# Performance work log

Measured on AMD Instinct MI355X. Metric: run time of the kernel, lower is better.

Reference implementation:

```python
import jax, jax.numpy as jnp
import numpy as np

D_MODEL = 1024
N_HEADS = 16


def setup_inputs() -> dict:
    key = jax.random.key(0)
    ks = jax.random.split(key, 7)
    scale = 1.0 / np.sqrt(D_MODEL)
    seq = jax.random.normal(ks[0], (4, 1024, D_MODEL), dtype=jnp.float32)
    Wq = jax.random.normal(ks[1], (D_MODEL, D_MODEL), dtype=jnp.float32) * scale
    bq = jax.random.normal(ks[2], (D_MODEL,), dtype=jnp.float32) * 0.02
    Wk = jax.random.normal(ks[3], (D_MODEL, D_MODEL), dtype=jnp.float32) * scale
    bk = jax.random.normal(ks[4], (D_MODEL,), dtype=jnp.float32) * 0.02
    Wv = jax.random.normal(ks[5], (D_MODEL, D_MODEL), dtype=jnp.float32) * scale
    bv = jax.random.normal(ks[6], (D_MODEL,), dtype=jnp.float32) * 0.02
    return {"seq": seq, "Wq": Wq, "bq": bq, "Wk": Wk, "bk": bk, "Wv": Wv, "bv": bv}


def reference(seq, Wq, bq, Wk, bk, Wv, bv):
    B, S, D = seq.shape
    H = N_HEADS
    dv = D // H
    # nn.Linear: x @ W.T + b; W stored [out, in]
    q = (seq @ Wq.T + bq).reshape(B, S, H, dv).transpose(0, 2, 1, 3)  # [B,H,S,dv]
    k = (seq @ Wk.T + bk).reshape(B, S, H, dv).transpose(0, 2, 1, 3)
    v = (seq @ Wv.T + bv).reshape(B, S, H, dv).transpose(0, 2, 1, 3)
    scores = jnp.einsum('bhqd,bhkd->bhqk', q, k) / jnp.sqrt(jnp.asarray(dv, seq.dtype))
    p = jax.nn.softmax(scores, axis=-1)
    out = jnp.einsum('bhqk,bhkd->bhqd', p, v)  # [B,H,S,dv]
    return out.transpose(0, 2, 1, 3).reshape(B, S, D)
```

## Files before the change

kernel.cpp:

```cpp
#include <hip/hip_runtime.h>
#include <hip/hip_fp16.h>

typedef _Float16 f16x8 __attribute__((ext_vector_type(8)));
typedef _Float16 f16x4 __attribute__((ext_vector_type(4)));
typedef float f32x4 __attribute__((ext_vector_type(4)));

#define D_MODEL 1024
#define SEQ 1024
#define BATCH 4
#define NH 16
#define DV 64
#define M_TOTAL (BATCH * SEQ)
#define QBLK 128

__device__ __forceinline__ void gload16(const _Float16* g, _Float16* lds) {
    __builtin_amdgcn_global_load_lds((const __attribute__((address_space(1))) void*)g,
                                     (__attribute__((address_space(3))) void*)lds,
                                     16, 0, 0);
}

__global__ void cvt_f32_f16(const float* __restrict__ s, _Float16* __restrict__ d, int n) {
    int i = (blockIdx.x * blockDim.x + threadIdx.x) * 8;
    if (i >= n) return;
    float4 a = *(const float4*)(s + i);
    float4 b = *(const float4*)(s + i + 4);
    f16x8 h;
    h[0] = (_Float16)a.x; h[1] = (_Float16)a.y; h[2] = (_Float16)a.z; h[3] = (_Float16)a.w;
    h[4] = (_Float16)b.x; h[5] = (_Float16)b.y; h[6] = (_Float16)b.z; h[7] = (_Float16)b.w;
    *(f16x8*)(d + i) = h;
}

__global__ void cvt3_f32_f16(const float* __restrict__ s0, const float* __restrict__ s1,
                             const float* __restrict__ s2, _Float16* __restrict__ d0,
                             _Float16* __restrict__ d1, _Float16* __restrict__ d2, int n) {
    const float* s = (blockIdx.y == 0) ? s0 : (blockIdx.y == 1 ? s1 : s2);
    _Float16*    d = (blockIdx.y == 0) ? d0 : (blockIdx.y == 1 ? d1 : d2);
    int i = (blockIdx.x * blockDim.x + threadIdx.x) * 8;
    if (i >= n) return;
    float4 a = *(const float4*)(s + i);
    float4 b = *(const float4*)(s + i + 4);
    f16x8 h;
    h[0] = (_Float16)a.x; h[1] = (_Float16)a.y; h[2] = (_Float16)a.z; h[3] = (_Float16)a.w;
    h[4] = (_Float16)b.x; h[5] = (_Float16)b.y; h[6] = (_Float16)b.z; h[7] = (_Float16)b.w;
    *(f16x8*)(d + i) = h;
}

__global__ __launch_bounds__(512, 2) void qkv_gemm(
    const _Float16* __restrict__ X,
    const _Float16* __restrict__ W0, const _Float16* __restrict__ W1, const _Float16* __restrict__ W2,
    const float* __restrict__ b0, const float* __restrict__ b1, const float* __restrict__ b2,
    _Float16* __restrict__ Qo, _Float16* __restrict__ Ko, _Float16* __restrict__ Vto)
{
    __shared__ _Float16 SM[4 * 256 * 64];
#define ABASE(buf) (SM + (buf) * 16384)
#define BBASE(buf) (SM + 32768 + (buf) * 16384)

    const int tid = threadIdx.x;
    const int l = tid & 63;
    const int w = tid >> 6;
    const int wr = w >> 2, wc = w & 3;

    const int bid = blockIdx.x;
    const int nid = (bid & 7) * 24 + (bid >> 3);
    const int mt = nid & 15, ntg = nid >> 4;
    const int mat = ntg >> 2, nt = ntg & 3;
    const _Float16* Wm  = (mat == 0) ? W0 : (mat == 1 ? W1 : W2);
    const float*    bia = (mat == 0) ? b0 : (mat == 1 ? b1 : b2);
    const int m0 = mt * 256, n0 = nt * 256;

    const int str = tid >> 3;
    const int sc8 = ((tid & 7) ^ (str & 7)) * 8;
    const _Float16* xsrc = X  + (size_t)(m0 + str) * D_MODEL + sc8;
    const _Float16* wsrc = Wm + (size_t)(n0 + str) * D_MODEL + sc8;
    const int ldst = str * 64 + (tid & 7) * 8;

#define SA(buf, kt, h) do { \
    gload16(xsrc + (size_t)((h) * 128) * D_MODEL + (kt) * 64, ABASE(buf) + (h) * 8192 + ldst); \
    gload16(xsrc + (size_t)((h) * 128 + 64) * D_MODEL + (kt) * 64, ABASE(buf) + (h) * 8192 + 4096 + ldst); } while (0)
#define SB(buf, kt, h) do { \
    gload16(wsrc + (size_t)((h) * 128) * D_MODEL + (kt) * 64, BBASE(buf) + (h) * 8192 + ldst); \
    gload16(wsrc + (size_t)((h) * 128 + 64) * D_MODEL + (kt) * 64, BBASE(buf) + (h) * 8192 + 4096 + ldst); } while (0)

    const int fr = l & 15, g = l >> 4, fr7 = l & 7;
    const int wrow = wr * 128, bcol = wc * 64;

    f32x4 acc[8][4] = {};
    f16x8 b[4][2];

    SB(0, 0, 0); SB(0, 0, 1);
    SA(0, 0, 0); SA(0, 0, 1);
    SB(1, 1, 0); SB(1, 1, 1);
    asm volatile("s_waitcnt vmcnt(4)" ::: "memory");
    __builtin_amdgcn_s_barrier();

#define PHASES(BUF, TSA_BUF, TSA, TSB_BUF, TSB)                                              \
    _Pragma("unroll")                                                                        \
    for (int p = 0; p < 4; ++p) {                                                            \
        if (p == 0) {                                                                        \
            _Pragma("unroll")                                                                \
            for (int nj = 0; nj < 4; ++nj) {                                                 \
                const int rb = (bcol + nj * 16 + fr) * 64;                                   \
                b[nj][0] = *(const f16x8*)&BBASE(BUF)[rb + ((g ^ fr7) << 3)];                \
                b[nj][1] = *(const f16x8*)&BBASE(BUF)[rb + (((4 + g) ^ fr7) << 3)];          \
            }                                                                                \
        }                                                                                    \
        f16x8 aq[2][2];                                                                      \
        _Pragma("unroll")                                                                    \
        for (int q = 0; q < 2; ++q) {                                                        \
            const int ra = (wrow + (2 * p + q) * 16 + fr) * 64;                              \
            aq[q][0] = *(const f16x8*)&ABASE(BUF)[ra + ((g ^ fr7) << 3)];                    \
            aq[q][1] = *(const f16x8*)&ABASE(BUF)[ra + (((4 + g) ^ fr7) << 3)];              \
        }                                                                                    \
        if (p == 0) SA(TSA_BUF, TSA, 0);                                                     \
        else if (p == 1) SA(TSA_BUF, TSA, 1);                                                \
        else if (p == 2) SB(TSB_BUF, TSB, 0);                                                \
        else SB(TSB_BUF, TSB, 1);                                                            \
        __builtin_amdgcn_s_barrier();                                                        \
        __builtin_amdgcn_s_setprio(1);                                                       \
        _Pragma("unroll")                                                                    \
        for (int ks = 0; ks < 2; ++ks)                                                       \
            _Pragma("unroll")                                                                \
            for (int q = 0; q < 2; ++q)                                                      \
                _Pragma("unroll")                                                            \
                for (int nj = 0; nj < 4; ++nj)                                               \
                    acc[2 * p + q][nj] = __builtin_amdgcn_mfma_f32_16x16x32_f16(             \
                        aq[q][ks], b[nj][ks], acc[2 * p + q][nj], 0, 0, 0);                  \
        __builtin_amdgcn_s_setprio(0);                                                       \
        if (p == 3) asm volatile("s_waitcnt vmcnt(4)" ::: "memory");                         \
        __builtin_amdgcn_s_barrier();                                                        \
    }

    for (int it = 0; it < 8; ++it) {
        const int tA = 2 * it + 1;
        const int tN = (2 * it + 2 < 16) ? 2 * it + 2 : 15;
        const int tM = (2 * it + 3 < 16) ? 2 * it + 3 : 15;
        PHASES(0, 1, tA, 0, tN)
        PHASES(1, 0, tN, 1, tM)
    }
#undef PHASES
#undef SA
#undef SB

    if (mat != 2) {
        const float scale = (mat == 0) ? 0.125f * 1.44269504088896340736f : 1.0f;
#pragma unroll
        for (int nj = 0; nj < 4; ++nj) {
            const int o = n0 + bcol + nj * 16 + fr;
            const float bb = bia[o];
            const int h = o >> 6, dd = o & 63;
#pragma unroll
            for (int mi = 0; mi < 8; ++mi) {
#pragma unroll
                for (int r = 0; r < 4; ++r) {
                    const int m = m0 + wrow + mi * 16 + g * 4 + r;
                    const int bi = m >> 10, s = m & 1023;
                    const float v = (acc[mi][nj][r] + bb) * scale;
                    const _Float16 hv = (_Float16)v;
                    const int bh = bi * NH + h;
                    if (mat == 0) Qo[((size_t)bh * SEQ + s) * DV + dd] = hv;
                    else          Ko[((size_t)bh * SEQ + s) * DV + dd] = hv;
                }
            }
        }
    } else {
        asm volatile("s_waitcnt vmcnt(0)" ::: "memory");
        __syncthreads();
#pragma unroll
        for (int nj = 0; nj < 4; ++nj) {
            const int n = bcol + nj * 16 + fr;
            const float bb = bia[n0 + n];
#pragma unroll
            for (int mi = 0; mi < 8; ++mi) {
#pragma unroll
                for (int r = 0; r < 4; ++r) {
                    const int m = wrow + mi * 16 + g * 4 + r;
                    SM[n * 256 + ((((m >> 3) + n) & 31) << 3) + (m & 7)] =
                        (_Float16)(acc[mi][nj][r] + bb);
                }
            }
        }
        __syncthreads();
        const int bi = m0 >> 10, s0 = m0 & 1023;
#pragma unroll
        for (int itp = 0; itp < 16; ++itp) {
            const int task = itp * 512 + tid;
            const int dd = task >> 5, sc = task & 31;
            f16x8 vv = *(const f16x8*)&SM[dd * 256 + (((sc + dd) & 31) << 3)];
            const int og = n0 + dd;
            const int h = og >> 6, d = og & 63;
            const int bh = bi * NH + h;
            *(f16x8*)(Vto + ((size_t)bh * DV + d) * SEQ + s0 + sc * 8) = vv;
        }
    }
#undef ABASE
#undef BBASE
}

__global__ __launch_bounds__(512, 4) void attn(
    const _Float16* __restrict__ Q, const _Float16* __restrict__ K,
    const _Float16* __restrict__ Vt, float* __restrict__ out)
{
    __shared__ _Float16 Kb[2][64 * 64];
    __shared__ _Float16 Vb[2][64 * 64];
    __shared__ _Float16 P[8][16][80];

    const int tid = threadIdx.x;
    const int w = tid >> 6, l = tid & 63;
    const int qc = l & 15, g = l >> 4;

    const int fid = blockIdx.y * 8 + blockIdx.x;
    const int nid = (fid & 7) * 64 + (fid >> 3);
    const int bh = nid >> 3, qt = nid & 7;
    const int b = bh >> 4, h = bh & 15;
    const int q0 = qt * QBLK + w * 16;

    const int str = tid >> 3;
    const int scs = ((tid & 7) ^ (str & 7)) * 8;
    const int ldst = str * 64 + (tid & 7) * 8;
    const _Float16* Kg = K  + (size_t)bh * SEQ * DV;
    const _Float16* Vg = Vt + (size_t)bh * DV * SEQ;

    const _Float16* qp = Q + ((size_t)bh * SEQ + q0 + qc) * DV + g * 8;
    f16x8 qf0 = *(const f16x8*)(qp);
    f16x8 qf1 = *(const f16x8*)(qp + 32);

    float m_run = -1e30f, l_run = 0.f;
    f32x4 oacc[4] = {};

#define STAGE(buf, kb) do {                                                  \
        gload16(Kg + (size_t)((kb) + str) * DV + scs, &Kb[buf][0] + ldst);   \
        gload16(Vg + (size_t)str * SEQ + (kb) + scs, &Vb[buf][0] + ldst);    \
    } while (0)

    STAGE(0, 0);
    __syncthreads();

    for (int kt = 0; kt < 16; ++kt) {
        const int ct = kt & 1;
        if (kt < 15) STAGE(ct ^ 1, (kt + 1) * 64);
        const _Float16* Ktile = Kb[ct];
        const _Float16* Vtile = Vb[ct];

        f32x4 sT[4];
        const f32x4 zf = {0.f, 0.f, 0.f, 0.f};
        __builtin_amdgcn_s_setprio(1);
#pragma unroll
        for (int kf = 0; kf < 4; ++kf) {
            const int row = kf * 16 + qc;
            f16x8 ka0 = *(const f16x8*)&Ktile[row * 64 + (((g)     ^ (qc & 7)) << 3)];
            f16x8 ka1 = *(const f16x8*)&Ktile[row * 64 + (((4 + g) ^ (qc & 7)) << 3)];
            f32x4 t = __builtin_amdgcn_mfma_f32_16x16x32_f16(ka0, qf0, zf, 0, 0, 0);
            sT[kf] = __builtin_amdgcn_mfma_f32_16x16x32_f16(ka1, qf1, t, 0, 0, 0);
        }
        __builtin_amdgcn_s_setprio(0);

        f32x4 mx = sT[0];
#pragma unroll
        for (int kf = 1; kf < 4; ++kf)
#pragma unroll
            for (int r = 0; r < 4; ++r) mx[r] = fmaxf(mx[r], sT[kf][r]);
        float pmax = fmaxf(fmaxf(mx[0], mx[1]), fmaxf(mx[2], mx[3]));
        pmax = fmaxf(pmax, __shfl_xor(pmax, 16));
        pmax = fmaxf(pmax, __shfl_xor(pmax, 32));
        if (!__all(pmax - m_run <= 8.0f)) {
            const float mn = fmaxf(m_run, pmax);
            const float al = exp2f(m_run - mn);
            l_run *= al;
#pragma unroll
            for (int df = 0; df < 4; ++df) oacc[df] *= al;
            m_run = mn;
        }
        float rsum = 0.f;
#pragma unroll
        for (int kf = 0; kf < 4; ++kf) {
            f16x4 ph;
#pragma unroll
            for (int r = 0; r < 4; ++r) {
                const float p = exp2f(sT[kf][r] - m_run);
                rsum += p;
                ph[r] = (_Float16)p;
            }
            *(f16x4*)&P[w][qc][kf * 16 + g * 4] = ph;
        }
        rsum += __shfl_xor(rsum, 16);
        rsum += __shfl_xor(rsum, 32);
        l_run += rsum;

        __builtin_amdgcn_s_setprio(1);
#pragma unroll
        for (int ks = 0; ks < 2; ++ks) {
            f16x8 pb = *(const f16x8*)&P[w][qc][ks * 32 + g * 8];
#pragma unroll
            for (int df = 0; df < 4; ++df) {
                const int row = df * 16 + qc;
                f16x8 va = *(const f16x8*)&Vtile[row * 64 + (((ks * 4 + g) ^ (qc & 7)) << 3)];
                oacc[df] = __builtin_amdgcn_mfma_f32_16x16x32_f16(va, pb, oacc[df], 0, 0, 0);
            }
        }
        __builtin_amdgcn_s_setprio(0);

        __syncthreads();
    }
#undef STAGE

    const float inv = 1.0f / l_run;
    float* ob = out + ((size_t)b * SEQ + q0 + qc) * D_MODEL + h * DV;
#pragma unroll
    for (int df = 0; df < 4; ++df) {
        float4 v4;
        v4.x = oacc[df][0] * inv; v4.y = oacc[df][1] * inv;
        v4.z = oacc[df][2] * inv; v4.w = oacc[df][3] * inv;
        *(float4*)(ob + df * 16 + g * 4) = v4;
    }
}

extern "C" void kernel_launch(void* const* d_in, const int* in_sizes, int n_in,
                              void* d_out, int out_size, void* d_ws, size_t ws_size,
                              hipStream_t stream) {
    const float* seq = (const float*)d_in[0];
    const float* Wq  = (const float*)d_in[1];
    const float* bq  = (const float*)d_in[2];
    const float* Wk  = (const float*)d_in[3];
    const float* bk  = (const float*)d_in[4];
    const float* Wv  = (const float*)d_in[5];
    const float* bv  = (const float*)d_in[6];
    float* out = (float*)d_out;

    _Float16* seqh = (_Float16*)d_ws;
    _Float16* wqh  = seqh + (size_t)M_TOTAL * D_MODEL;
    _Float16* wkh  = wqh + (size_t)D_MODEL * D_MODEL;
    _Float16* wvh  = wkh + (size_t)D_MODEL * D_MODEL;
    _Float16* Qh   = wvh + (size_t)D_MODEL * D_MODEL;
    _Float16* Kh   = Qh + (size_t)M_TOTAL * D_MODEL;
    _Float16* Vth  = Kh + (size_t)M_TOTAL * D_MODEL;

    const int n_seq = M_TOTAL * D_MODEL;
    const int n_w   = D_MODEL * D_MODEL;
    cvt_f32_f16<<<n_seq / (256 * 8), 256, 0, stream>>>(seq, seqh, n_seq);
    cvt3_f32_f16<<<dim3(n_w / (256 * 8), 3), 256, 0, stream>>>(Wq, Wk, Wv, wqh, wkh, wvh, n_w);

    qkv_gemm<<<192, 512, 0, stream>>>(
        seqh, wqh, wkh, wvh, bq, bk, bv, Qh, Kh, Vth);

    attn<<<dim3(SEQ / QBLK, BATCH * NH), 512, 0, stream>>>(Qh, Kh, Vth, out);
}
```

Before: 84.31 us.

## Software-pipeline attention loop: overlap next QK^T with current softmax/PV using triple buffering

Restructures the attention inner loop so the QK^T MFMAs for tile t+1 are issued before the softmax and PV for tile t, using two score register sets and a three-slot K/V LDS ring. The aim is to hide the latency of exp, reductions and LDS round trips behind matrix-core work, and to keep loads two tiles ahead. In exchange it uses more LDS (an extra K and V buffer) and more registers for the second score set, which may reduce occupancy under launch_bounds(512,4). It also adds explicit vmcnt(0) waits before each barrier.

After: 82.46 us. 2.2% less time.

```diff
diff --git a/kernel.cpp b/kernel.cpp
--- a/kernel.cpp
+++ b/kernel.cpp
@@ -200,8 +200,8 @@
     const _Float16* __restrict__ Q, const _Float16* __restrict__ K,
     const _Float16* __restrict__ Vt, float* __restrict__ out)
 {
-    __shared__ _Float16 Kb[2][64 * 64];
-    __shared__ _Float16 Vb[2][64 * 64];
+    __shared__ _Float16 Kb[3][64 * 64];
+    __shared__ _Float16 Vb[3][64 * 64];
     __shared__ _Float16 P[8][16][80];
 
     const int tid = threadIdx.x;
@@ -226,82 +226,104 @@
 
     float m_run = -1e30f, l_run = 0.f;
     f32x4 oacc[4] = {};
-
-#define STAGE(buf, kb) do {                                                  \
-        gload16(Kg + (size_t)((kb) + str) * DV + scs, &Kb[buf][0] + ldst);   \
-        gload16(Vg + (size_t)str * SEQ + (kb) + scs, &Vb[buf][0] + ldst);    \
+    const f32x4 zf = {0.f, 0.f, 0.f, 0.f};
+
+#define STAGE(buf, kt) do {                                                    \
+        gload16(Kg + (size_t)((kt) * 64 + str) * DV + scs, &Kb[buf][0] + ldst);\
+        gload16(Vg + (size_t)str * SEQ + (kt) * 64 + scs, &Vb[buf][0] + ldst); \
     } while (0)
 
+#define QK(S, kbuf) do {                                                                    \
+        __builtin_amdgcn_s_setprio(1);                                                      \
+        _Pragma("unroll")                                                                   \
+        for (int kf = 0; kf < 4; ++kf) {                                                    \
+            const int row = kf * 16 + qc;                                                   \
+            f16x8 ka0 = *(const f16x8*)&Kb[kbuf][row * 64 + (((g)     ^ (qc & 7)) << 3)];   \
+            f16x8 ka1 = *(const f16x8*)&Kb[kbuf][row * 64 + (((4 + g) ^ (qc & 7)) << 3)];   \
+            f32x4 tt = __builtin_amdgcn_mfma_f32_16x16x32_f16(ka0, qf0, zf, 0, 0, 0);       \
+            S[kf] = __builtin_amdgcn_mfma_f32_16x16x32_f16(ka1, qf1, tt, 0, 0, 0);          \
+        }                                                                                   \
+        __builtin_amdgcn_s_setprio(0);                                                      \
+    } while (0)
+
+#define SOFTPV(S, vbuf) do {                                                                \
+        f32x4 mx = S[0];                                                                    \
+        _Pragma("unroll")                                                                   \
+        for (int kf = 1; kf < 4; ++kf)                                                      \
+            _Pragma("unroll")                                                               \
+            for (int r = 0; r < 4; ++r) mx[r] = fmaxf(mx[r], S[kf][r]);                     \
+        float pmax = fmaxf(fmaxf(mx[0], mx[1]), fmaxf(mx[2], mx[3]));                       \
+        pmax = fmaxf(pmax, __shfl_xor(pmax, 16));                                           \
+        pmax = fmaxf(pmax, __shfl_xor(pmax, 32));                                           \
+        if (!__all(pmax - m_run <= 8.0f)) {                                                 \
+            const float mn = fmaxf(m_run, pmax);                                            \
+            const float al = exp2f(m_run - mn);                                             \
+            l_run *= al;                                                                    \
+            _Pragma("unroll")                                                               \
+            for (int df = 0; df < 4; ++df) oacc[df] *= al;                                  \
+            m_run = mn;                                                                     \
+        }                                                                                   \
+        float rsum = 0.f;                                                                   \
+        _Pragma("unroll")                                                                   \
+        for (int kf = 0; kf < 4; ++kf) {                                                    \
+            f16x4 ph;                                                                       \
+            _Pragma("unroll")                                                               \
+            for (int r = 0; r < 4; ++r) {                                                   \
+                const float p = exp2f(S[kf][r] - m_run);                                    \
+                rsum += p;                                                                  \
+                ph[r] = (_Float16)p;                                                        \
+            }                                                                               \
+            *(f16x4*)&P[w][qc][kf * 16 + g * 4] = ph;                                       \
+        }                                                                                   \
+        rsum += __shfl_xor(rsum, 16);                                                       \
+        rsum += __shfl_xor(rsum, 32);                                                       \
+        l_run += rsum;                                                                      \
+        __builtin_amdgcn_s_setprio(1);                                                      \
+        _Pragma("unroll")                                                                   \
+        for (int ks = 0; ks < 2; ++ks) {                                                    \
+            f16x8 pb = *(const f16x8*)&P[w][qc][ks * 32 + g * 8];                           \
+            _Pragma("unroll")                                                               \
+            for (int df = 0; df < 4; ++df) {                                                \
+                const int row = df * 16 + qc;                                               \
+                f16x8 va = *(const f16x8*)&Vb[vbuf][row * 64 +                              \
+                                                    (((ks * 4 + g) ^ (qc & 7)) << 3)];      \
+                oacc[df] = __builtin_amdgcn_mfma_f32_16x16x32_f16(va, pb, oacc[df], 0,0,0); \
+            }                                                                               \
+        }                                                                                   \
+        __builtin_amdgcn_s_setprio(0);                                                      \
+    } while (0)
+
+    f32x4 sA[4], sB[4];
+
     STAGE(0, 0);
+    asm volatile("s_waitcnt vmcnt(0)" ::: "memory");
     __syncthreads();
-
-    for (int kt = 0; kt < 16; ++kt) {
-        const int ct = kt & 1;
-        if (kt < 15) STAGE(ct ^ 1, (kt + 1) * 64);
-        const _Float16* Ktile = Kb[ct];
-        const _Float16* Vtile = Vb[ct];
-
-        f32x4 sT[4];
-        const f32x4 zf = {0.f, 0.f, 0.f, 0.f};
-        __builtin_amdgcn_s_setprio(1);
-#pragma unroll
-        for (int kf = 0; kf < 4; ++kf) {
-            const int row = kf * 16 + qc;
-            f16x8 ka0 = *(const f16x8*)&Ktile[row * 64 + (((g)     ^ (qc & 7)) << 3)];
-            f16x8 ka1 = *(const f16x8*)&Ktile[row * 64 + (((4 + g) ^ (qc & 7)) << 3)];
-            f32x4 t = __builtin_amdgcn_mfma_f32_16x16x32_f16(ka0, qf0, zf, 0, 0, 0);
-            sT[kf] = __builtin_amdgcn_mfma_f32_16x16x32_f16(ka1, qf1, t, 0, 0, 0);
-        }
-        __builtin_amdgcn_s_setprio(0);
-
-        f32x4 mx = sT[0];
-#pragma unroll
-        for (int kf = 1; kf < 4; ++kf)
-#pragma unroll
-            for (int r = 0; r < 4; ++r) mx[r] = fmaxf(mx[r], sT[kf][r]);
-        float pmax = fmaxf(fmaxf(mx[0], mx[1]), fmaxf(mx[2], mx[3]));
-        pmax = fmaxf(pmax, __shfl_xor(pmax, 16));
-        pmax = fmaxf(pmax, __shfl_xor(pmax, 32));
-        if (!__all(pmax - m_run <= 8.0f)) {
-            const float mn = fmaxf(m_run, pmax);
-            const float al = exp2f(m_run - mn);
-            l_run *= al;
-#pragma unroll
-            for (int df = 0; df < 4; ++df) oacc[df] *= al;
-            m_run = mn;
-        }
-        float rsum = 0.f;
-#pragma unroll
-        for (int kf = 0; kf < 4; ++kf) {
-            f16x4 ph;
-#pragma unroll
-            for (int r = 0; r < 4; ++r) {
-                const float p = exp2f(sT[kf][r] - m_run);
-                rsum += p;
-                ph[r] = (_Float16)p;
-            }
-            *(f16x4*)&P[w][qc][kf * 16 + g * 4] = ph;
-        }
-        rsum += __shfl_xor(rsum, 16);
-        rsum += __shfl_xor(rsum, 32);
-        l_run += rsum;
-
-        __builtin_amdgcn_s_setprio(1);
-#pragma unroll
-        for (int ks = 0; ks < 2; ++ks) {
-            f16x8 pb = *(const f16x8*)&P[w][qc][ks * 32 + g * 8];
-#pragma unroll
-            for (int df = 0; df < 4; ++df) {
-                const int row = df * 16 + qc;
-                f16x8 va = *(const f16x8*)&Vtile[row * 64 + (((ks * 4 + g) ^ (qc & 7)) << 3)];
-                oacc[df] = __builtin_amdgcn_mfma_f32_16x16x32_f16(va, pb, oacc[df], 0, 0, 0);
-            }
-        }
-        __builtin_amdgcn_s_setprio(0);
-
+    STAGE(1, 1);
+    QK(sA, 0);
+    asm volatile("s_waitcnt vmcnt(0)" ::: "memory");
+    __syncthreads();
+
+#pragma unroll
+    for (int it = 0; it < 7; ++it) {
+        const int t1 = 2 * it + 1, t2 = 2 * it + 2;
+        STAGE((t1 + 1) % 3, t1 + 1);
+        QK(sB, t1 % 3);
+        SOFTPV(sA, (t1 - 1) % 3);
+        asm volatile("s_waitcnt vmcnt(0)" ::: "memory");
         __syncthreads();
-    }
+        STAGE((t2 + 1) % 3, t2 + 1);
+        QK(sA, t2 % 3);
+        SOFTPV(sB, (t2 - 1) % 3);
+        asm volatile("s_waitcnt vmcnt(0)" ::: "memory");
+        __syncthreads();
+    }
+    QK(sB, 15 % 3);
+    SOFTPV(sA, 14 % 3);
+    SOFTPV(sB, 15 % 3);
+
 #undef STAGE
+#undef QK
+#undef SOFTPV
 
     const float inv = 1.0f / l_run;
     float* ob = out + ((size_t)b * SEQ + q0 + qc) * D_MODEL + h * DV;
```

## Triple-buffer K/V tiles in attention with explicit vmcnt waits

Applied to the files above, without the earlier changes.

Moves the attention kernel's K/V LDS staging from double to triple buffering, prefetching two tiles ahead. A fixed s_waitcnt vmcnt count replaces the full __syncthreads drain, so loads stay in flight across iterations. LDS use grows by 16KB per block, which may reduce occupancy at 4 blocks/CU. The extra prefetch at the tail redundantly reloads tile 15.

Result: no change. 84.98 us (+0.8%).

```diff
diff --git a/kernel.cpp b/kernel.cpp
--- a/kernel.cpp
+++ b/kernel.cpp
@@ -200,8 +200,8 @@
     const _Float16* __restrict__ Q, const _Float16* __restrict__ K,
     const _Float16* __restrict__ Vt, float* __restrict__ out)
 {
-    __shared__ _Float16 Kb[2][64 * 64];
-    __shared__ _Float16 Vb[2][64 * 64];
+    __shared__ _Float16 Kb[3][64 * 64];
+    __shared__ _Float16 Vb[3][64 * 64];
     __shared__ _Float16 P[8][16][80];
 
     const int tid = threadIdx.x;
@@ -226,31 +226,36 @@
 
     float m_run = -1e30f, l_run = 0.f;
     f32x4 oacc[4] = {};
-
-#define STAGE(buf, kb) do {                                                  \
-        gload16(Kg + (size_t)((kb) + str) * DV + scs, &Kb[buf][0] + ldst);   \
-        gload16(Vg + (size_t)str * SEQ + (kb) + scs, &Vb[buf][0] + ldst);    \
+    const f32x4 zf = {0.f, 0.f, 0.f, 0.f};
+
+#define STAGE(slot, kt) do {                                                      \
+        gload16(Kg + (size_t)((kt) * 64 + str) * DV + scs, &Kb[slot][0] + ldst);  \
+        gload16(Vg + (size_t)str * SEQ + (kt) * 64 + scs, &Vb[slot][0] + ldst);   \
     } while (0)
 
     STAGE(0, 0);
-    __syncthreads();
-
-    for (int kt = 0; kt < 16; ++kt) {
-        const int ct = kt & 1;
-        if (kt < 15) STAGE(ct ^ 1, (kt + 1) * 64);
-        const _Float16* Ktile = Kb[ct];
-        const _Float16* Vtile = Vb[ct];
+    STAGE(1, 1);
+    asm volatile("s_waitcnt vmcnt(2)" ::: "memory");
+    __builtin_amdgcn_s_barrier();
+
+    for (int t = 0; t < 16; ++t) {
+        const int cs_ = t % 3;
+        const int ns  = (t + 2) % 3;
+        const int tn  = (t + 2 < 16) ? t + 2 : 15;
+        STAGE(ns, tn);
+        asm volatile("s_waitcnt vmcnt(4)" ::: "memory");
+        __builtin_amdgcn_s_barrier();
+        __builtin_amdgcn_sched_barrier(0);
 
         f32x4 sT[4];
-        const f32x4 zf = {0.f, 0.f, 0.f, 0.f};
         __builtin_amdgcn_s_setprio(1);
 #pragma unroll
         for (int kf = 0; kf < 4; ++kf) {
             const int row = kf * 16 + qc;
-            f16x8 ka0 = *(const f16x8*)&Ktile[row * 64 + (((g)     ^ (qc & 7)) << 3)];
-            f16x8 ka1 = *(const f16x8*)&Ktile[row * 64 + (((4 + g) ^ (qc & 7)) << 3)];
-            f32x4 t = __builtin_amdgcn_mfma_f32_16x16x32_f16(ka0, qf0, zf, 0, 0, 0);
-            sT[kf] = __builtin_amdgcn_mfma_f32_16x16x32_f16(ka1, qf1, t, 0, 0, 0);
+            f16x8 ka0 = *(const f16x8*)&Kb[cs_][row * 64 + (((g)     ^ (qc & 7)) << 3)];
+            f16x8 ka1 = *(const f16x8*)&Kb[cs_][row * 64 + (((4 + g) ^ (qc & 7)) << 3)];
+            f32x4 tt = __builtin_amdgcn_mfma_f32_16x16x32_f16(ka0, qf0, zf, 0, 0, 0);
+            sT[kf] = __builtin_amdgcn_mfma_f32_16x16x32_f16(ka1, qf1, tt, 0, 0, 0);
         }
         __builtin_amdgcn_s_setprio(0);
 
@@ -293,15 +298,18 @@
 #pragma unroll
             for (int df = 0; df < 4; ++df) {
                 const int row = df * 16 + qc;
-                f16x8 va = *(const f16x8*)&Vtile[row * 64 + (((ks * 4 + g) ^ (qc & 7)) << 3)];
+                f16x8 va = *(const f16x8*)&Vb[cs_][row * 64 + (((ks * 4 + g) ^ (qc & 7)) << 3)];
                 oacc[df] = __builtin_amdgcn_mfma_f32_16x16x32_f16(va, pb, oacc[df], 0, 0, 0);
             }
         }
         __builtin_amdgcn_s_setprio(0);
 
-        __syncthreads();
+        __builtin_amdgcn_sched_barrier(0);
+        __builtin_amdgcn_s_barrier();
     }
 #undef STAGE
+
+    asm volatile("s_waitcnt vmcnt(0)" ::: "memory");
 
     const float inv = 1.0f / l_run;
     float* ob = out + ((size_t)b * SEQ + q0 + qc) * D_MODEL + h * DV;
```

## Load V fragments directly from global to registers and defer row-sum reduction

Applied to the files above, without the earlier changes.

The attention kernel no longer stages V tiles in shared memory. Each wave loads its V MFMA operands straight from global memory into registers, split into two halves that are issued around the QK^T MFMAs to hide latency. The per-tile cross-lane row-sum shuffles are moved after the loop, and the max shuffles now run only on the rescale path. Occupancy bounds rise from 4 to 6 to use the freed LDS. The cost is that V is now read redundantly by each of the 8 waves through global/L2 rather than once per block, and register pressure rises under a tighter launch bound.

Measured after the change: 134.3 us. 59.3% more time.

```diff
diff --git a/kernel.cpp b/kernel.cpp
--- a/kernel.cpp
+++ b/kernel.cpp
@@ -196,12 +196,11 @@
 #undef BBASE
 }
 
-__global__ __launch_bounds__(512, 4) void attn(
+__global__ __launch_bounds__(512, 6) void attn(
     const _Float16* __restrict__ Q, const _Float16* __restrict__ K,
     const _Float16* __restrict__ Vt, float* __restrict__ out)
 {
     __shared__ _Float16 Kb[2][64 * 64];
-    __shared__ _Float16 Vb[2][64 * 64];
     __shared__ _Float16 P[8][16][80];
 
     const int tid = threadIdx.x;
@@ -226,43 +225,49 @@
 
     float m_run = -1e30f, l_run = 0.f;
     f32x4 oacc[4] = {};
-
-#define STAGE(buf, kb) do {                                                  \
-        gload16(Kg + (size_t)((kb) + str) * DV + scs, &Kb[buf][0] + ldst);   \
-        gload16(Vg + (size_t)str * SEQ + (kb) + scs, &Vb[buf][0] + ldst);    \
-    } while (0)
-
-    STAGE(0, 0);
+    const f32x4 zf = {0.f, 0.f, 0.f, 0.f};
+
+#define KSTAGE(buf, kt) gload16(Kg + (size_t)((kt) * 64 + str) * DV + scs, &Kb[buf][0] + ldst)
+
+    KSTAGE(0, 0);
     __syncthreads();
 
-    for (int kt = 0; kt < 16; ++kt) {
-        const int ct = kt & 1;
-        if (kt < 15) STAGE(ct ^ 1, (kt + 1) * 64);
-        const _Float16* Ktile = Kb[ct];
-        const _Float16* Vtile = Vb[ct];
+    for (int t = 0; t < 16; ++t) {
+        const int ct = t & 1;
+        const int kb = t * 64;
+        if (t < 15) KSTAGE(ct ^ 1, t + 1);
+
+        f16x8 vr0[4], vr1[4];
+#pragma unroll
+        for (int df = 0; df < 4; ++df)
+            vr0[df] = *(const f16x8*)(Vg + (size_t)(df * 16 + qc) * SEQ + kb + g * 8);
 
         f32x4 sT[4];
-        const f32x4 zf = {0.f, 0.f, 0.f, 0.f};
         __builtin_amdgcn_s_setprio(1);
 #pragma unroll
         for (int kf = 0; kf < 4; ++kf) {
             const int row = kf * 16 + qc;
-            f16x8 ka0 = *(const f16x8*)&Ktile[row * 64 + (((g)     ^ (qc & 7)) << 3)];
-            f16x8 ka1 = *(const f16x8*)&Ktile[row * 64 + (((4 + g) ^ (qc & 7)) << 3)];
-            f32x4 t = __builtin_amdgcn_mfma_f32_16x16x32_f16(ka0, qf0, zf, 0, 0, 0);
-            sT[kf] = __builtin_amdgcn_mfma_f32_16x16x32_f16(ka1, qf1, t, 0, 0, 0);
+            f16x8 ka0 = *(const f16x8*)&Kb[ct][row * 64 + (((g)     ^ (qc & 7)) << 3)];
+            f16x8 ka1 = *(const f16x8*)&Kb[ct][row * 64 + (((4 + g) ^ (qc & 7)) << 3)];
+            f32x4 tt = __builtin_amdgcn_mfma_f32_16x16x32_f16(ka0, qf0, zf, 0, 0, 0);
+            sT[kf] = __builtin_amdgcn_mfma_f32_16x16x32_f16(ka1, qf1, tt, 0, 0, 0);
         }
         __builtin_amdgcn_s_setprio(0);
 
+#pragma unroll
+        for (int df = 0; df < 4; ++df)
+            vr1[df] = *(const f16x8*)(Vg + (size_t)(df * 16 + qc) * SEQ + kb + 32 + g * 8);
+
         f32x4 mx = sT[0];
 #pragma unroll
         for (int kf = 1; kf < 4; ++kf)
 #pragma unroll
             for (int r = 0; r < 4; ++r) mx[r] = fmaxf(mx[r], sT[kf][r]);
-        float pmax = fmaxf(fmaxf(mx[0], mx[1]), fmaxf(mx[2], mx[3]));
-        pmax = fmaxf(pmax, __shfl_xor(pmax, 16));
-        pmax = fmaxf(pmax, __shfl_xor(pmax, 32));
-        if (!__all(pmax - m_run <= 8.0f)) {
+        const float lmax = fmaxf(fmaxf(mx[0], mx[1]), fmaxf(mx[2], mx[3]));
+        if (!__all(lmax - m_run <= 8.0f)) {
+            float pmax = lmax;
+            pmax = fmaxf(pmax, __shfl_xor(pmax, 16));
+            pmax = fmaxf(pmax, __shfl_xor(pmax, 32));
             const float mn = fmaxf(m_run, pmax);
             const float al = exp2f(m_run - mn);
             l_run *= al;
@@ -282,27 +287,27 @@
             }
             *(f16x4*)&P[w][qc][kf * 16 + g * 4] = ph;
         }
-        rsum += __shfl_xor(rsum, 16);
-        rsum += __shfl_xor(rsum, 32);
         l_run += rsum;
 
         __builtin_amdgcn_s_setprio(1);
-#pragma unroll
-        for (int ks = 0; ks < 2; ++ks) {
-            f16x8 pb = *(const f16x8*)&P[w][qc][ks * 32 + g * 8];
-#pragma unroll
-            for (int df = 0; df < 4; ++df) {
-                const int row = df * 16 + qc;
-                f16x8 va = *(const f16x8*)&Vtile[row * 64 + (((ks * 4 + g) ^ (qc & 7)) << 3)];
-                oacc[df] = __builtin_amdgcn_mfma_f32_16x16x32_f16(va, pb, oacc[df], 0, 0, 0);
-            }
+        {
+            f16x8 pb0 = *(const f16x8*)&P[w][qc][g * 8];
+#pragma unroll
+            for (int df = 0; df < 4; ++df)
+                oacc[df] = __builtin_amdgcn_mfma_f32_16x16x32_f16(vr0[df], pb0, oacc[df], 0, 0, 0);
+            f16x8 pb1 = *(const f16x8*)&P[w][qc][32 + g * 8];
+#pragma unroll
+            for (int df = 0; df < 4; ++df)
+                oacc[df] = __builtin_amdgcn_mfma_f32_16x16x32_f16(vr1[df], pb1, oacc[df], 0, 0, 0);
         }
         __builtin_amdgcn_s_setprio(0);
 
         __syncthreads();
     }
-#undef STAGE
-
+#undef KSTAGE
+
+    l_run += __shfl_xor(l_run, 16);
+    l_run += __shfl_xor(l_run, 32);
     const float inv = 1.0f / l_run;
     float* ob = out + ((size_t)b * SEQ + q0 + qc) * D_MODEL + h * DV;
 #pragma unroll
```
